# Performance work log

Measured on AMD Instinct MI355X. Metric: run time of the kernel, lower is better.

The kernel has to match this reference:

```python
import jax, jax.numpy as jnp
import numpy as np

B, S, DIM = 32, 1, 2048
N_HEADS, N_KV = 32, 8
HEAD_DIM = DIM // N_HEADS  # 64
MAXB, MAXS = 32, 2048
START_POS = 2047
THETA = 10000.0  # precompute_freqs_cis called without theta -> llama default


def setup_inputs() -> dict:
    key = jax.random.key(0)
    ks = jax.random.split(key, 7)
    u = lambda k, s: jax.random.uniform(k, s, jnp.float32) * 0.02  # scaled torch.rand init
    return {
        "x": jax.random.normal(ks[0], (B, S, DIM), jnp.float32),
        "q_w": u(ks[1], (DIM, N_HEADS * HEAD_DIM)),
        "k_w": u(ks[2], (DIM, N_KV * HEAD_DIM)),
        "v_w": u(ks[3], (DIM, N_KV * HEAD_DIM)),
        "o_w": u(ks[4], (DIM, N_HEADS * HEAD_DIM)),
        "cache_k": jax.random.normal(ks[5], (MAXB, MAXS, N_KV, HEAD_DIM), jnp.float32) * 0.02,
        "cache_v": jax.random.normal(ks[6], (MAXB, MAXS, N_KV, HEAD_DIM), jnp.float32) * 0.02,
        "start_pos": START_POS,
    }


def _rope(x, cos, sin):
    # x: [B, S, H, D]; consecutive pairs (even, odd) form complex numbers (llama view_as_complex)
    xr, xi = x[..., 0::2], x[..., 1::2]
    out = jnp.stack([xr * cos - xi * sin, xr * sin + xi * cos], axis=-1)
    return out.reshape(x.shape)


def _attn_fwd(x, q_w, k_w, v_w, o_w, cache_k, cache_v, start_pos):
    B_, S_, _ = x.shape
    # fused_linear(x, W) == x @ W
    xq = (x @ q_w).reshape(B_, S_, N_HEADS, HEAD_DIM)
    xk = (x @ k_w).reshape(B_, S_, N_KV, HEAD_DIM)
    xv = (x @ v_w).reshape(B_, S_, N_KV, HEAD_DIM)

    # RoPE freqs for positions [start_pos, start_pos + S)
    inv = 1.0 / (THETA ** (jnp.arange(0, HEAD_DIM, 2, dtype=jnp.float32) / HEAD_DIM))
    t = jnp.arange(start_pos, start_pos + S_, dtype=jnp.float32)
    ang = t[:, None] * inv[None, :]                    # [S, D/2]
    cos = jnp.cos(ang)[None, :, None, :]               # [1, S, 1, D/2]
    sin = jnp.sin(ang)[None, :, None, :]
    xq = _rope(xq, cos, sin)
    xk = _rope(xk, cos, sin)

    # KV-cache append
    cache_k = jax.lax.dynamic_update_slice(cache_k, xk, (0, start_pos, 0, 0))
    cache_v = jax.lax.dynamic_update_slice(cache_v, xv, (0, start_pos, 0, 0))
    L = start_pos + S_
    keys = cache_k[:B_, :L].transpose(0, 2, 1, 3)      # [B, Hkv, L, D]
    vals = cache_v[:B_, :L].transpose(0, 2, 1, 3)

    # GQA attention; grouped einsum = repeat_kv without materializing copies
    rep = N_HEADS // N_KV
    q = xq.transpose(0, 2, 1, 3).reshape(B_, N_KV, rep, S_, HEAD_DIM)
    scores = jnp.einsum('bkrsd,bkld->bkrsl', q, keys) * (HEAD_DIM ** -0.5)
    p = jax.nn.softmax(scores, axis=-1)
    o = jnp.einsum('bkrsl,bkld->bkrsd', p, vals)
    o = o.reshape(B_, N_HEADS, S_, HEAD_DIM).transpose(0, 2, 1, 3).reshape(B_, S_, -1)
    return o @ o_w


def reference(x, q_w, k_w, v_w, o_w, cache_k, cache_v, start_pos):
    return _attn_fwd(x, q_w, k_w, v_w, o_w, cache_k, cache_v, start_pos)
```

## Files before the change

kernel.cpp:

```cpp
#include <hip/hip_runtime.h>
#include <hip/hip_bf16.h>
#include <math.h>

#define NQKV 3072

__device__ __forceinline__ int read_sp(const int* spp) {
  if (!spp) return 2047;
  int raw = spp[0];
  if (raw >= 0 && raw < 2048) return raw;
  union { int i; float f; } u; u.i = raw;
  if (u.f >= 0.f && u.f < 2048.f) return (int)u.f;
  return 2047;
}

__global__ __launch_bounds__(256) void k_prep(const float* __restrict__ x,
                                              float* __restrict__ xt) {
  int idx = blockIdx.x * 256 + threadIdx.x;
  int r = idx >> 11, k = idx & 2047;
  xt[k * 32 + r] = x[idx];
}

__global__ __launch_bounds__(256) void k_qkv(const float* __restrict__ qw,
                                             const float* __restrict__ kw,
                                             const float* __restrict__ vw,
                                             const float* __restrict__ xt,
                                             float* __restrict__ part, int kc) {
  int colb = blockIdx.x, j = blockIdx.y;
  int n = colb * 256 + threadIdx.x;
  const float* w; int ldw, nn;
  if (colb < 8)       { w = qw; ldw = 2048; nn = n; }
  else if (colb < 10) { w = kw; ldw = 512;  nn = n - 2048; }
  else                { w = vw; ldw = 512;  nn = n - 2560; }
  int k0 = j * kc;
  const float* wp = w + (size_t)k0 * ldw + nn;
  float acc[32];
  #pragma unroll
  for (int r = 0; r < 32; r++) acc[r] = 0.f;
  #pragma unroll 2
  for (int kk = 0; kk < kc; kk++) {
    float wv = wp[(size_t)kk * ldw];
    const float* xr = xt + (size_t)(k0 + kk) * 32;
    #pragma unroll
    for (int r = 0; r < 32; r++) acc[r] = fmaf(xr[r], wv, acc[r]);
  }
  float* po = part + (size_t)j * 32 * NQKV + n;
  #pragma unroll
  for (int r = 0; r < 32; r++) po[(size_t)r * NQKV] = acc[r];
}

__global__ __launch_bounds__(1024) void k_attn(const float* __restrict__ ck,
                                               const float* __restrict__ cv,
                                               const float* __restrict__ part,
                                               float* __restrict__ obt,
                                               const int* __restrict__ spp,
                                               int ks) {
  int h = blockIdx.x, b = blockIdx.y, tid = threadIdx.x;
  int sp = read_sp(spp);

  __shared__ float qraw[384];
  __shared__ __align__(16) float qs[4][64];
  __shared__ __align__(16) float knew[64];
  __shared__ __align__(16) float vnew[64];
  __shared__ __align__(16) float sc[4][2048];
  __shared__ float wredm[16][4];
  __shared__ float wred[16];
  __shared__ float mfin[4];
  __shared__ float inv_[4];
  __shared__ __align__(16) float opart[16][4][64];

  if (tid < 384) {
    int col;
    if (tid < 256)      col = h * 256 + tid;
    else if (tid < 320) col = 2048 + h * 64 + (tid - 256);
    else                col = 2560 + h * 64 + (tid - 320);
    float s = 0.f;
    for (int j = 0; j < ks; j++) s += part[(size_t)(j * 32 + b) * NQKV + col];
    qraw[tid] = s;
  }
  __syncthreads();

  if (tid < 160) {
    int rr = tid >> 5, i = tid & 31;
    double freq = pow(10000.0, -(double)(2 * i) / 64.0);
    double ang = (double)sp * freq;
    double sd, cd; sincos(ang, &sd, &cd);
    float sn = (float)sd, cs = (float)cd;
    if (rr < 4) {
      float a = qraw[rr * 64 + 2 * i], bq = qraw[rr * 64 + 2 * i + 1];
      qs[rr][2 * i]     = (a * cs - bq * sn) * 0.125f;
      qs[rr][2 * i + 1] = (a * sn + bq * cs) * 0.125f;
    } else {
      float a = qraw[256 + 2 * i], bk = qraw[256 + 2 * i + 1];
      knew[2 * i]     = a * cs - bk * sn;
      knew[2 * i + 1] = a * sn + bk * cs;
    }
  } else if (tid < 224) {
    vnew[tid - 160] = qraw[320 + (tid - 160)];
  }
  __syncthreads();

  int w   = tid >> 6;
  int lane = tid & 63;
  int pp  = lane >> 4;
  int d4  = lane & 15;
  int base = w * 128;

  float4 qv0 = *(const float4*)&qs[0][d4 * 4];
  float4 qv1 = *(const float4*)&qs[1][d4 * 4];
  float4 qv2 = *(const float4*)&qs[2][d4 * 4];
  float4 qv3 = *(const float4*)&qs[3][d4 * 4];
  float4 kn4 = *(const float4*)&knew[d4 * 4];
  float4 vn4 = *(const float4*)&vnew[d4 * 4];

  const float* kb = ck + ((size_t)b * 2048 * 8 + h) * 64;
  float lm0 = -1e30f, lm1 = -1e30f, lm2 = -1e30f, lm3 = -1e30f;
  #pragma unroll 4
  for (int i = 0; i < 32; i++) {
    int p = base + i * 4 + pp;
    float4 k4 = *(const float4*)(kb + (size_t)p * 512 + d4 * 4);
    if (p == sp) k4 = kn4;
    float s0 = qv0.x * k4.x + qv0.y * k4.y + qv0.z * k4.z + qv0.w * k4.w;
    float s1 = qv1.x * k4.x + qv1.y * k4.y + qv1.z * k4.z + qv1.w * k4.w;
    float s2 = qv2.x * k4.x + qv2.y * k4.y + qv2.z * k4.z + qv2.w * k4.w;
    float s3 = qv3.x * k4.x + qv3.y * k4.y + qv3.z * k4.z + qv3.w * k4.w;
    #pragma unroll
    for (int off = 1; off <= 8; off <<= 1) {
      s0 += __shfl_xor(s0, off);
      s1 += __shfl_xor(s1, off);
      s2 += __shfl_xor(s2, off);
      s3 += __shfl_xor(s3, off);
    }
    lm0 = fmaxf(lm0, s0); lm1 = fmaxf(lm1, s1);
    lm2 = fmaxf(lm2, s2); lm3 = fmaxf(lm3, s3);
    float sv = (d4 == 0) ? s0 : (d4 == 1) ? s1 : (d4 == 2) ? s2 : s3;
    if (d4 < 4) sc[d4][p] = sv;
  }
  lm0 = fmaxf(lm0, __shfl_xor(lm0, 16)); lm0 = fmaxf(lm0, __shfl_xor(lm0, 32));
  lm1 = fmaxf(lm1, __shfl_xor(lm1, 16)); lm1 = fmaxf(lm1, __shfl_xor(lm1, 32));
  lm2 = fmaxf(lm2, __shfl_xor(lm2, 16)); lm2 = fmaxf(lm2, __shfl_xor(lm2, 32));
  lm3 = fmaxf(lm3, __shfl_xor(lm3, 16)); lm3 = fmaxf(lm3, __shfl_xor(lm3, 32));
  if (lane == 0) {
    wredm[w][0] = lm0; wredm[w][1] = lm1; wredm[w][2] = lm2; wredm[w][3] = lm3;
  }
  __syncthreads();
  if (tid < 4) {
    float m = wredm[0][tid];
    #pragma unroll
    for (int w2 = 1; w2 < 16; w2++) m = fmaxf(m, wredm[w2][tid]);
    mfin[tid] = m;
  }
  __syncthreads();

  {
    int r = tid >> 8;
    int t = tid & 255;
    float m = mfin[r];
    float lsum = 0.f;
    #pragma unroll
    for (int jj = 0; jj < 8; jj++) {
      float e = __expf(sc[r][jj * 256 + t] - m);
      lsum += e;
      sc[r][jj * 256 + t] = e;
    }
    #pragma unroll
    for (int off = 32; off > 0; off >>= 1) lsum += __shfl_xor(lsum, off);
    if ((tid & 63) == 0) wred[w] = lsum;
  }
  __syncthreads();
  if (tid < 4)
    inv_[tid] = 1.0f / (wred[tid * 4 + 0] + wred[tid * 4 + 1] +
                        wred[tid * 4 + 2] + wred[tid * 4 + 3]);
  __syncthreads();

  const float* vb = cv + ((size_t)b * 2048 * 8 + h) * 64;
  float4 a0 = {0,0,0,0}, a1 = {0,0,0,0}, a2 = {0,0,0,0}, a3 = {0,0,0,0};
  #pragma unroll 4
  for (int i = 0; i < 32; i++) {
    int p = base + i * 4 + pp;
    float4 v4 = *(const float4*)(vb + (size_t)p * 512 + d4 * 4);
    if (p == sp) v4 = vn4;
    float e0 = sc[0][p], e1 = sc[1][p], e2 = sc[2][p], e3 = sc[3][p];
    a0.x = fmaf(e0, v4.x, a0.x); a0.y = fmaf(e0, v4.y, a0.y);
    a0.z = fmaf(e0, v4.z, a0.z); a0.w = fmaf(e0, v4.w, a0.w);
    a1.x = fmaf(e1, v4.x, a1.x); a1.y = fmaf(e1, v4.y, a1.y);
    a1.z = fmaf(e1, v4.z, a1.z); a1.w = fmaf(e1, v4.w, a1.w);
    a2.x = fmaf(e2, v4.x, a2.x); a2.y = fmaf(e2, v4.y, a2.y);
    a2.z = fmaf(e2, v4.z, a2.z); a2.w = fmaf(e2, v4.w, a2.w);
    a3.x = fmaf(e3, v4.x, a3.x); a3.y = fmaf(e3, v4.y, a3.y);
    a3.z = fmaf(e3, v4.z, a3.z); a3.w = fmaf(e3, v4.w, a3.w);
  }
  #pragma unroll
  for (int off = 16; off <= 32; off <<= 1) {
    a0.x += __shfl_xor(a0.x, off); a0.y += __shfl_xor(a0.y, off);
    a0.z += __shfl_xor(a0.z, off); a0.w += __shfl_xor(a0.w, off);
    a1.x += __shfl_xor(a1.x, off); a1.y += __shfl_xor(a1.y, off);
    a1.z += __shfl_xor(a1.z, off); a1.w += __shfl_xor(a1.w, off);
    a2.x += __shfl_xor(a2.x, off); a2.y += __shfl_xor(a2.y, off);
    a2.z += __shfl_xor(a2.z, off); a2.w += __shfl_xor(a2.w, off);
    a3.x += __shfl_xor(a3.x, off); a3.y += __shfl_xor(a3.y, off);
    a3.z += __shfl_xor(a3.z, off); a3.w += __shfl_xor(a3.w, off);
  }
  if (pp == 0) {
    *(float4*)&opart[w][0][d4 * 4] = a0;
    *(float4*)&opart[w][1][d4 * 4] = a1;
    *(float4*)&opart[w][2][d4 * 4] = a2;
    *(float4*)&opart[w][3][d4 * 4] = a3;
  }
  __syncthreads();
  if (tid < 256) {
    int rr = tid >> 6, dd = tid & 63;
    float o = 0.f;
    #pragma unroll
    for (int w2 = 0; w2 < 16; w2++) o += opart[w2][rr][dd];
    o *= inv_[rr];
    int col = (h * 4 + rr) * 64 + dd;
    obt[(size_t)col * 32 + b] = o;
  }
}

__global__ __launch_bounds__(256) void k_oproj(const float* __restrict__ ow,
                                               const float* __restrict__ obt,
                                               float* __restrict__ part, int kc) {
  int colb = blockIdx.x, j = blockIdx.y;
  int n = colb * 256 + threadIdx.x;
  int k0 = j * kc;
  const float* wp = ow + (size_t)k0 * 2048 + n;
  float acc[32];
  #pragma unroll
  for (int r = 0; r < 32; r++) acc[r] = 0.f;
  #pragma unroll 2
  for (int kk = 0; kk < kc; kk++) {
    float wv = wp[(size_t)kk * 2048];
    const float* xr = obt + (size_t)(k0 + kk) * 32;
    #pragma unroll
    for (int r = 0; r < 32; r++) acc[r] = fmaf(xr[r], wv, acc[r]);
  }
  float* po = part + (size_t)j * 32 * 2048 + n;
  #pragma unroll
  for (int r = 0; r < 32; r++) po[(size_t)r * 2048] = acc[r];
}

__global__ __launch_bounds__(256) void k_finish(const float* __restrict__ part,
                                                float* __restrict__ out, int ks) {
  int idx = blockIdx.x * 256 + threadIdx.x;
  float s = 0.f;
  for (int j = 0; j < ks; j++) s += part[(size_t)j * 65536 + idx];
  out[idx] = s;
}

extern "C" void kernel_launch(void* const* d_in, const int* in_sizes, int n_in,
                              void* d_out, int out_size, void* d_ws, size_t ws_size,
                              hipStream_t stream) {
  const float* x  = (const float*)d_in[0];
  const float* qw = (const float*)d_in[1];
  const float* kw = (const float*)d_in[2];
  const float* vw = (const float*)d_in[3];
  const float* ow = (const float*)d_in[4];
  const float* ck = (const float*)d_in[5];
  const float* cv = (const float*)d_in[6];
  const int*   sp = (n_in >= 8) ? (const int*)d_in[7] : nullptr;

  int ks = 1;
  {
    const int cands[4] = {16, 8, 4, 2};
    for (int i = 0; i < 4; i++) {
      if ((size_t)(131072 + (size_t)cands[i] * 98304) * 4 <= ws_size) { ks = cands[i]; break; }
    }
  }
  int kc = 2048 / ks;

  float* ws   = (float*)d_ws;
  float* xt   = ws;
  float* part = xt + 65536;
  float* obt  = part + (size_t)ks * 98304;
  float* part_out = part;

  k_prep  <<<256,          256,  0, stream>>>(x, xt);
  k_qkv   <<<dim3(12, ks), 256,  0, stream>>>(qw, kw, vw, xt, part, kc);
  k_attn  <<<dim3(8, 32),  1024, 0, stream>>>(ck, cv, part, obt, sp, ks);
  k_oproj <<<dim3(8, ks),  256,  0, stream>>>(ow, obt, part_out, kc);
  k_finish<<<256,          256,  0, stream>>>(part_out, (float*)d_out, ks);
}
```

Baseline: 390.4 us.

## Split attention over sequence chunks with flash-decoding combine and precomputed RoPE

Replaces the single 1024-thread attention block per (head-group, batch) with 8 sequence splits of 256 positions, each writing partial outputs plus max and sum, then merged in a new combine kernel. The q/k/v split-K partial sums are reduced once in a separate kernel, and the RoPE cos/sin table is computed once in the prep kernel instead of in double precision in every block. GEMM inner-loop unroll factors are raised from 2 to 8. The intent is more blocks and higher occupancy for the KV-cache-bound attention, at the cost of two extra launches and additional workspace traffic.

```diff
diff --git a/kernel.cpp b/kernel.cpp
--- a/kernel.cpp
+++ b/kernel.cpp
@@ -3,6 +3,8 @@
 #include <math.h>
 
 #define NQKV 3072
+#define NS 8
+#define SPL 256
 
 __device__ __forceinline__ int read_sp(const int* spp) {
   if (!spp) return 2047;
@@ -14,10 +16,21 @@
 }
 
 __global__ __launch_bounds__(256) void k_prep(const float* __restrict__ x,
-                                              float* __restrict__ xt) {
+                                              float* __restrict__ xt,
+                                              float* __restrict__ rope,
+                                              const int* __restrict__ spp) {
   int idx = blockIdx.x * 256 + threadIdx.x;
   int r = idx >> 11, k = idx & 2047;
   xt[k * 32 + r] = x[idx];
+  if (blockIdx.x == 0 && threadIdx.x < 32) {
+    int i = threadIdx.x;
+    int sp = read_sp(spp);
+    double freq = pow(10000.0, -(double)(2 * i) / 64.0);
+    double ang = (double)sp * freq;
+    double sd, cd; sincos(ang, &sd, &cd);
+    rope[2 * i]     = (float)cd;
+    rope[2 * i + 1] = (float)sd;
+  }
 }
 
 __global__ __launch_bounds__(256) void k_qkv(const float* __restrict__ qw,
@@ -36,7 +49,7 @@
   float acc[32];
   #pragma unroll
   for (int r = 0; r < 32; r++) acc[r] = 0.f;
-  #pragma unroll 2
+  #pragma unroll 8
   for (int kk = 0; kk < kc; kk++) {
     float wv = wp[(size_t)kk * ldw];
     const float* xr = xt + (size_t)(k0 + kk) * 32;
@@ -48,43 +61,48 @@
   for (int r = 0; r < 32; r++) po[(size_t)r * NQKV] = acc[r];
 }
 
-__global__ __launch_bounds__(1024) void k_attn(const float* __restrict__ ck,
-                                               const float* __restrict__ cv,
-                                               const float* __restrict__ part,
-                                               float* __restrict__ obt,
-                                               const int* __restrict__ spp,
-                                               int ks) {
-  int h = blockIdx.x, b = blockIdx.y, tid = threadIdx.x;
+__global__ __launch_bounds__(256) void k_qred(const float* __restrict__ part,
+                                              float* __restrict__ qred, int ks) {
+  int col = blockIdx.x * 256 + threadIdx.x;
+  int b = blockIdx.y;
+  float s = 0.f;
+  for (int j = 0; j < ks; j++) s += part[(size_t)(j * 32 + b) * NQKV + col];
+  qred[(size_t)b * NQKV + col] = s;
+}
+
+__global__ __launch_bounds__(256) void k_attn_split(const float* __restrict__ ck,
+                                                    const float* __restrict__ cv,
+                                                    const float* __restrict__ qred,
+                                                    const float* __restrict__ rope,
+                                                    float* __restrict__ osplit,
+                                                    float* __restrict__ msl,
+                                                    const int* __restrict__ spp) {
+  int h = blockIdx.x, b = blockIdx.y, s = blockIdx.z;
+  int tid = threadIdx.x;
   int sp = read_sp(spp);
 
   __shared__ float qraw[384];
   __shared__ __align__(16) float qs[4][64];
   __shared__ __align__(16) float knew[64];
   __shared__ __align__(16) float vnew[64];
-  __shared__ __align__(16) float sc[4][2048];
-  __shared__ float wredm[16][4];
-  __shared__ float wred[16];
+  __shared__ __align__(16) float sc[4][SPL];
+  __shared__ float wredm[4][4];
+  __shared__ float wred[4];
   __shared__ float mfin[4];
-  __shared__ float inv_[4];
-  __shared__ __align__(16) float opart[16][4][64];
-
-  if (tid < 384) {
+  __shared__ __align__(16) float opart[4][4][64];
+
+  for (int i = tid; i < 384; i += 256) {
     int col;
-    if (tid < 256)      col = h * 256 + tid;
-    else if (tid < 320) col = 2048 + h * 64 + (tid - 256);
-    else                col = 2560 + h * 64 + (tid - 320);
-    float s = 0.f;
-    for (int j = 0; j < ks; j++) s += part[(size_t)(j * 32 + b) * NQKV + col];
-    qraw[tid] = s;
+    if (i < 256)      col = h * 256 + i;
+    else if (i < 320) col = 2048 + h * 64 + (i - 256);
+    else              col = 2560 + h * 64 + (i - 320);
+    qraw[i] = qred[(size_t)b * NQKV + col];
   }
   __syncthreads();
 
   if (tid < 160) {
     int rr = tid >> 5, i = tid & 31;
-    double freq = pow(10000.0, -(double)(2 * i) / 64.0);
-    double ang = (double)sp * freq;
-    double sd, cd; sincos(ang, &sd, &cd);
-    float sn = (float)sd, cs = (float)cd;
+    float cs = rope[2 * i], sn = rope[2 * i + 1];
     if (rr < 4) {
       float a = qraw[rr * 64 + 2 * i], bq = qraw[rr * 64 + 2 * i + 1];
       qs[rr][2 * i]     = (a * cs - bq * sn) * 0.125f;
@@ -99,11 +117,11 @@
   }
   __syncthreads();
 
-  int w   = tid >> 6;
+  int w    = tid >> 6;
   int lane = tid & 63;
-  int pp  = lane >> 4;
-  int d4  = lane & 15;
-  int base = w * 128;
+  int pp   = lane >> 4;
+  int d4   = lane & 15;
+  int base = s * SPL + w * 64;
 
   float4 qv0 = *(const float4*)&qs[0][d4 * 4];
   float4 qv1 = *(const float4*)&qs[1][d4 * 4];
@@ -114,8 +132,8 @@
 
   const float* kb = ck + ((size_t)b * 2048 * 8 + h) * 64;
   float lm0 = -1e30f, lm1 = -1e30f, lm2 = -1e30f, lm3 = -1e30f;
-  #pragma unroll 4
-  for (int i = 0; i < 32; i++) {
+  #pragma unroll
+  for (int i = 0; i < 16; i++) {
     int p = base + i * 4 + pp;
     float4 k4 = *(const float4*)(kb + (size_t)p * 512 + d4 * 4);
     if (p == sp) k4 = kn4;
@@ -133,7 +151,7 @@
     lm0 = fmaxf(lm0, s0); lm1 = fmaxf(lm1, s1);
     lm2 = fmaxf(lm2, s2); lm3 = fmaxf(lm3, s3);
     float sv = (d4 == 0) ? s0 : (d4 == 1) ? s1 : (d4 == 2) ? s2 : s3;
-    if (d4 < 4) sc[d4][p] = sv;
+    if (d4 < 4) sc[d4][w * 64 + i * 4 + pp] = sv;
   }
   lm0 = fmaxf(lm0, __shfl_xor(lm0, 16)); lm0 = fmaxf(lm0, __shfl_xor(lm0, 32));
   lm1 = fmaxf(lm1, __shfl_xor(lm1, 16)); lm1 = fmaxf(lm1, __shfl_xor(lm1, 32));
@@ -143,43 +161,42 @@
     wredm[w][0] = lm0; wredm[w][1] = lm1; wredm[w][2] = lm2; wredm[w][3] = lm3;
   }
   __syncthreads();
-  if (tid < 4) {
-    float m = wredm[0][tid];
-    #pragma unroll
-    for (int w2 = 1; w2 < 16; w2++) m = fmaxf(m, wredm[w2][tid]);
-    mfin[tid] = m;
-  }
+  if (tid < 4)
+    mfin[tid] = fmaxf(fmaxf(wredm[0][tid], wredm[1][tid]),
+                      fmaxf(wredm[2][tid], wredm[3][tid]));
   __syncthreads();
 
   {
-    int r = tid >> 8;
-    int t = tid & 255;
+    int r = w, t = lane;
     float m = mfin[r];
     float lsum = 0.f;
     #pragma unroll
-    for (int jj = 0; jj < 8; jj++) {
-      float e = __expf(sc[r][jj * 256 + t] - m);
+    for (int jj = 0; jj < 4; jj++) {
+      float e = __expf(sc[r][jj * 64 + t] - m);
       lsum += e;
-      sc[r][jj * 256 + t] = e;
+      sc[r][jj * 64 + t] = e;
     }
     #pragma unroll
     for (int off = 32; off > 0; off >>= 1) lsum += __shfl_xor(lsum, off);
-    if ((tid & 63) == 0) wred[w] = lsum;
-  }
-  __syncthreads();
-  if (tid < 4)
-    inv_[tid] = 1.0f / (wred[tid * 4 + 0] + wred[tid * 4 + 1] +
-                        wred[tid * 4 + 2] + wred[tid * 4 + 3]);
-  __syncthreads();
+    if (lane == 0) wred[r] = lsum;
+  }
+  __syncthreads();
+
+  if (tid < 4) {
+    size_t idx = (((size_t)(h * 32 + b) * NS + s) * 4 + tid) * 2;
+    msl[idx]     = mfin[tid];
+    msl[idx + 1] = wred[tid];
+  }
 
   const float* vb = cv + ((size_t)b * 2048 * 8 + h) * 64;
   float4 a0 = {0,0,0,0}, a1 = {0,0,0,0}, a2 = {0,0,0,0}, a3 = {0,0,0,0};
-  #pragma unroll 4
-  for (int i = 0; i < 32; i++) {
+  #pragma unroll
+  for (int i = 0; i < 16; i++) {
     int p = base + i * 4 + pp;
     float4 v4 = *(const float4*)(vb + (size_t)p * 512 + d4 * 4);
     if (p == sp) v4 = vn4;
-    float e0 = sc[0][p], e1 = sc[1][p], e2 = sc[2][p], e3 = sc[3][p];
+    int pl = w * 64 + i * 4 + pp;
+    float e0 = sc[0][pl], e1 = sc[1][pl], e2 = sc[2][pl], e3 = sc[3][pl];
     a0.x = fmaf(e0, v4.x, a0.x); a0.y = fmaf(e0, v4.y, a0.y);
     a0.z = fmaf(e0, v4.z, a0.z); a0.w = fmaf(e0, v4.w, a0.w);
     a1.x = fmaf(e1, v4.x, a1.x); a1.y = fmaf(e1, v4.y, a1.y);
@@ -207,15 +224,37 @@
     *(float4*)&opart[w][3][d4 * 4] = a3;
   }
   __syncthreads();
-  if (tid < 256) {
+  {
     int rr = tid >> 6, dd = tid & 63;
-    float o = 0.f;
-    #pragma unroll
-    for (int w2 = 0; w2 < 16; w2++) o += opart[w2][rr][dd];
-    o *= inv_[rr];
-    int col = (h * 4 + rr) * 64 + dd;
-    obt[(size_t)col * 32 + b] = o;
-  }
+    float o = opart[0][rr][dd] + opart[1][rr][dd] +
+              opart[2][rr][dd] + opart[3][rr][dd];
+    osplit[(((size_t)(h * 32 + b) * NS + s) * 4 + rr) * 64 + dd] = o;
+  }
+}
+
+__global__ __launch_bounds__(256) void k_combine(const float* __restrict__ osplit,
+                                                 const float* __restrict__ msl,
+                                                 float* __restrict__ obt) {
+  int h = blockIdx.x, b = blockIdx.y;
+  int tid = threadIdx.x;
+  int r = tid >> 6, d = tid & 63;
+  float ml[NS], ll[NS];
+  float m = -1e30f;
+  #pragma unroll
+  for (int s2 = 0; s2 < NS; s2++) {
+    size_t idx = (((size_t)(h * 32 + b) * NS + s2) * 4 + r) * 2;
+    ml[s2] = msl[idx]; ll[s2] = msl[idx + 1];
+    m = fmaxf(m, ml[s2]);
+  }
+  float L = 0.f, o = 0.f;
+  #pragma unroll
+  for (int s2 = 0; s2 < NS; s2++) {
+    float wgt = __expf(ml[s2] - m);
+    L = fmaf(wgt, ll[s2], L);
+    o = fmaf(wgt, osplit[(((size_t)(h * 32 + b) * NS + s2) * 4 + r) * 64 + d], o);
+  }
+  int col = (h * 4 + r) * 64 + d;
+  obt[(size_t)col * 32 + b] = o / L;
 }
 
 __global__ __launch_bounds__(256) void k_oproj(const float* __restrict__ ow,
@@ -228,7 +267,7 @@
   float acc[32];
   #pragma unroll
   for (int r = 0; r < 32; r++) acc[r] = 0.f;
-  #pragma unroll 2
+  #pragma unroll 8
   for (int kk = 0; kk < kc; kk++) {
     float wv = wp[(size_t)kk * 2048];
     const float* xr = obt + (size_t)(k0 + kk) * 32;
@@ -260,24 +299,31 @@
   const float* cv = (const float*)d_in[6];
   const int*   sp = (n_in >= 8) ? (const int*)d_in[7] : nullptr;
 
+  const size_t FIXED = 65536 + 65536 + 98304 + 524288 + 16384 + 64;
   int ks = 1;
   {
     const int cands[4] = {16, 8, 4, 2};
     for (int i = 0; i < 4; i++) {
-      if ((size_t)(131072 + (size_t)cands[i] * 98304) * 4 <= ws_size) { ks = cands[i]; break; }
+      if ((FIXED + (size_t)cands[i] * 98304) * 4 <= ws_size) { ks = cands[i]; break; }
     }
   }
   int kc = 2048 / ks;
 
-  float* ws   = (float*)d_ws;
-  float* xt   = ws;
-  float* part = xt + 65536;
-  float* obt  = part + (size_t)ks * 98304;
+  float* ws     = (float*)d_ws;
+  float* xt     = ws;
+  float* part   = xt + 65536;
+  float* obt    = part + (size_t)ks * 98304;
+  float* qred   = obt + 65536;
+  float* osplit = qred + 98304;
+  float* msl    = osplit + 524288;
+  float* rope   = msl + 16384;
   float* part_out = part;
 
-  k_prep  <<<256,          256,  0, stream>>>(x, xt);
-  k_qkv   <<<dim3(12, ks), 256,  0, stream>>>(qw, kw, vw, xt, part, kc);
-  k_attn  <<<dim3(8, 32),  1024, 0, stream>>>(ck, cv, part, obt, sp, ks);
-  k_oproj <<<dim3(8, ks),  256,  0, stream>>>(ow, obt, part_out, kc);
-  k_finish<<<256,          256,  0, stream>>>(part_out, (float*)d_out, ks);
-}
+  k_prep      <<<256,              256, 0, stream>>>(x, xt, rope, sp);
+  k_qkv       <<<dim3(12, ks),     256, 0, stream>>>(qw, kw, vw, xt, part, kc);
+  k_qred      <<<dim3(12, 32),     256, 0, stream>>>(part, qred, ks);
+  k_attn_split<<<dim3(8, 32, NS),  256, 0, stream>>>(ck, cv, qred, rope, osplit, msl, sp);
+  k_combine   <<<dim3(8, 32),      256, 0, stream>>>(osplit, msl, obt);
+  k_oproj     <<<dim3(8, ks),      256, 0, stream>>>(ow, obt, part_out, kc);
+  k_finish    <<<256,              256, 0, stream>>>(part_out, (float*)d_out, ks);
+}
```

New measurement: 391.3 us. No clear change (+0.2%).
